# Kernel tuning notes

Hardware: AMD Instinct MI355X
Metric: run time of the kernel (lower is better)

The kernel has to match this reference:

```python
import jax, jax.numpy as jnp
import numpy as np

N, E, G = 50000, 800000, 512
EMB, HID, NSHAPE, NCOLOR, NCLS = 128, 256, 64, 64, 32


def setup_inputs() -> dict:
    key = jax.random.key(0)
    ks = jax.random.split(key, 12)
    s = 0.05
    return {
        "x": jax.random.randint(ks[0], (N, 2), 0, NSHAPE),
        "edge_index": jax.random.randint(ks[1], (2, E), 0, N),
        "batch": jnp.sort(jax.random.randint(ks[2], (N,), 0, G)),
        "shape_emb": jax.random.normal(ks[3], (NSHAPE, EMB)) * s,
        "color_emb": jax.random.normal(ks[4], (NCOLOR, EMB)) * s,
        # SAGEConv: lin_l (applied to aggregated neighbors, with bias), lin_r (root, no bias)
        "w1l": jax.random.normal(ks[5], (HID, 2 * EMB)) * s,
        "b1l": jnp.zeros((HID,)),
        "w1r": jax.random.normal(ks[6], (HID, 2 * EMB)) * s,
        "w2l": jax.random.normal(ks[7], (HID, HID)) * s,
        "b2l": jnp.zeros((HID,)),
        "w2r": jax.random.normal(ks[8], (HID, HID)) * s,
        "wc": jax.random.normal(ks[9], (NCLS, HID)) * s,
        "bc": jnp.zeros((NCLS,)),
    }


def _sage_conv(h, src, dst, wl, bl, wr):
    # mean-aggregate messages h[src] onto dst, then lin_l(aggr) + lin_r(h)
    msg = h[src]  # [E, d]
    agg = jax.ops.segment_sum(msg, dst, num_segments=N)  # [N, d]
    deg = jax.ops.segment_sum(jnp.ones((src.shape[0],), h.dtype), dst, num_segments=N)
    agg = agg / jnp.maximum(deg, 1.0)[:, None]
    return agg @ wl.T + bl + h @ wr.T


def reference(x, edge_index, batch, shape_emb, color_emb,
              w1l, b1l, w1r, w2l, b2l, w2r, wc, bc):
    src, dst = edge_index[0], edge_index[1]
    h = jnp.concatenate([shape_emb[x[:, 0]], color_emb[x[:, 1]]], axis=-1)  # [N, 2*EMB]
    h = jax.nn.relu(_sage_conv(h, src, dst, w1l, b1l, w1r))
    h = jax.nn.relu(_sage_conv(h, src, dst, w2l, b2l, w2r))
    # global mean pool over graphs
    hs = jax.ops.segment_sum(h, batch, num_segments=G)  # [G, HID]
    cnt = jax.ops.segment_sum(jnp.ones((N,), h.dtype), batch, num_segments=G)
    hg = hs / jnp.maximum(cnt, 1.0)[:, None]
    return hg @ wc.T + bc  # [G, NCLS]
```

## Files before the change

### kernel.cpp

```cpp
#include <hip/hip_runtime.h>
#include <hip/hip_bf16.h>


#define EMB   128
#define HID   256
#define NCLS  32
#define DIM   256

typedef __attribute__((ext_vector_type(8))) short short8v;
typedef __attribute__((ext_vector_type(4))) float float4v;

__device__ __forceinline__ unsigned short f2bf(float f) {
    unsigned int u = __float_as_uint(f);
    unsigned int r = u + 0x7FFFu + ((u >> 16) & 1u);
    return (unsigned short)(r >> 16);
}
__device__ __forceinline__ float bf2f(unsigned short s) {
    return __uint_as_float(((unsigned int)s) << 16);
}

__global__ void build_bq(const float* __restrict__ wl, const float* __restrict__ wr,
                         unsigned short* __restrict__ bhi, unsigned short* __restrict__ blo) {
    int tid = blockIdx.x * 256 + threadIdx.x;
    int k = tid >> 8, o = tid & 255;
    float v = (k < 256) ? wl[o * 256 + k] : wr[o * 256 + (k - 256)];
    unsigned short h = f2bf(v);
    unsigned short l = f2bf(v - bf2f(h));
    int idx = (((k >> 3) * 256) + o) * 8 + (k & 7);
    bhi[idx] = h;
    blo[idx] = l;
}

__global__ void embed_bf16(const int* __restrict__ x,
                           const float* __restrict__ se, const float* __restrict__ ce,
                           unsigned short* __restrict__ hb, int n_nodes) {
    int tid = blockIdx.x * 256 + threadIdx.x;
    if (tid >= n_nodes * 32) return;
    int n = tid >> 5, c = tid & 31;
    const float* src = (c < 16) ? (se + (size_t)x[n * 2] * EMB + c * 8)
                                : (ce + (size_t)x[n * 2 + 1] * EMB + (c - 16) * 8);
    float4 v0 = *(const float4*)src;
    float4 v1 = *(const float4*)(src + 4);
    ushort4 o0 = make_ushort4(f2bf(v0.x), f2bf(v0.y), f2bf(v0.z), f2bf(v0.w));
    ushort4 o1 = make_ushort4(f2bf(v1.x), f2bf(v1.y), f2bf(v1.z), f2bf(v1.w));
    *(ushort4*)(hb + (size_t)tid * 8)     = o0;
    *(ushort4*)(hb + (size_t)tid * 8 + 4) = o1;
}


__global__ void count_deg(const int* __restrict__ dst, int* __restrict__ deg, int E) {
    int e = blockIdx.x * 256 + threadIdx.x;
    if (e < E) atomicAdd(&deg[dst[e]], 1);
}

__global__ void scan_block(const int* __restrict__ deg, int* __restrict__ rowptr,
                           int* __restrict__ bsums, int n) {
    __shared__ int s[256];
    int t = threadIdx.x;
    int i = blockIdx.x * 256 + t;
    int v = (i < n) ? deg[i] : 0;
    s[t] = v; __syncthreads();
    for (int off = 1; off < 256; off <<= 1) {
        int x = (t >= off) ? s[t - off] : 0;
        __syncthreads(); s[t] += x; __syncthreads();
    }
    if (i < n) rowptr[i] = s[t] - v;
    if (t == 255) bsums[blockIdx.x] = s[255];
}

__global__ void scan_sums(int* __restrict__ bsums, int nb, int* __restrict__ rowptr,
                          int n, int E) {
    __shared__ int s[256];
    int t = threadIdx.x;
    int v = (t < nb) ? bsums[t] : 0;
    s[t] = v; __syncthreads();
    for (int off = 1; off < 256; off <<= 1) {
        int x = (t >= off) ? s[t - off] : 0;
        __syncthreads(); s[t] += x; __syncthreads();
    }
    if (t < nb) bsums[t] = s[t] - v;
    if (t == 0) rowptr[n] = E;
}

__global__ void scan_add(int* __restrict__ rowptr, const int* __restrict__ bsums, int n) {
    int i = blockIdx.x * 256 + threadIdx.x;
    if (i < n) rowptr[i] += bsums[i >> 8];
}

__global__ void fill_csr(const int* __restrict__ src, const int* __restrict__ dst,
                         const int* __restrict__ rowptr, int* __restrict__ cursor,
                         int* __restrict__ csr, int E) {
    int e = blockIdx.x * 256 + threadIdx.x;
    if (e >= E) return;
    int d = dst[e];
    int pos = rowptr[d] + atomicAdd(&cursor[d], 1);
    csr[pos] = src[e];
}

__global__ void aggregate_bf16(const unsigned short* __restrict__ hb,
                               const int* __restrict__ rowptr, const int* __restrict__ csr,
                               float* __restrict__ agg, int n_nodes) {
    int wid = (blockIdx.x * 256 + threadIdx.x) >> 6;
    int lane = threadIdx.x & 63;
    if (wid >= n_nodes) return;
    int beg = rowptr[wid], end = rowptr[wid + 1];
    float a0 = 0.f, a1 = 0.f, a2 = 0.f, a3 = 0.f;
    int k = beg;
    for (; k + 3 < end; k += 4) {
        int s0 = csr[k], s1 = csr[k + 1], s2 = csr[k + 2], s3 = csr[k + 3];
        ushort4 u0 = *(const ushort4*)(hb + (size_t)s0 * DIM + lane * 4);
        ushort4 u1 = *(const ushort4*)(hb + (size_t)s1 * DIM + lane * 4);
        ushort4 u2 = *(const ushort4*)(hb + (size_t)s2 * DIM + lane * 4);
        ushort4 u3 = *(const ushort4*)(hb + (size_t)s3 * DIM + lane * 4);
        a0 += bf2f(u0.x) + bf2f(u1.x) + bf2f(u2.x) + bf2f(u3.x);
        a1 += bf2f(u0.y) + bf2f(u1.y) + bf2f(u2.y) + bf2f(u3.y);
        a2 += bf2f(u0.z) + bf2f(u1.z) + bf2f(u2.z) + bf2f(u3.z);
        a3 += bf2f(u0.w) + bf2f(u1.w) + bf2f(u2.w) + bf2f(u3.w);
    }
    for (; k < end; ++k) {
        ushort4 u = *(const ushort4*)(hb + (size_t)csr[k] * DIM + lane * 4);
        a0 += bf2f(u.x); a1 += bf2f(u.y); a2 += bf2f(u.z); a3 += bf2f(u.w);
    }
    int d = end - beg;
    float inv = 1.0f / (float)(d > 1 ? d : 1);
    float4 o; o.x = a0 * inv; o.y = a1 * inv; o.z = a2 * inv; o.w = a3 * inv;
    *(float4*)(agg + (size_t)wid * DIM + lane * 4) = o;
}

__global__ void __launch_bounds__(256)
gemm_mfma(const float* __restrict__ Agg, const unsigned short* __restrict__ Hinb,
          const unsigned short* __restrict__ Bhi, const unsigned short* __restrict__ Blo,
          const float* __restrict__ bias,
          float* __restrict__ Houtf, unsigned short* __restrict__ Houtb, int M) {
    __shared__ __align__(16) unsigned short As_hi[64 * 40];
    __shared__ __align__(16) unsigned short As_lo[64 * 40];

    const int t = threadIdx.x;
    const int w = t >> 6, lane = t & 63;
    const int lrow = lane & 15, koct = lane >> 4;
    const int nw = w * 64;
    const int m0 = blockIdx.x * 64;

    float4v acc[4][4];
#pragma unroll
    for (int i = 0; i < 4; ++i)
#pragma unroll
        for (int j = 0; j < 4; ++j) acc[i][j] = (float4v){0.f, 0.f, 0.f, 0.f};

    const int sr = t >> 2;
    const int sc = (t & 3) * 8;
    const int gr = m0 + sr;
    const bool valid = (gr < M);

#pragma unroll 1
    for (int kt = 0; kt < 8; ++kt) {
        const float* __restrict__ Ap = Agg + (size_t)gr * DIM + (kt * 32 + sc);
        float4 v0 = make_float4(0.f, 0.f, 0.f, 0.f), v1 = v0;
        if (valid) { v0 = *(const float4*)Ap; v1 = *(const float4*)(Ap + 4); }
        float fv[8] = {v0.x, v0.y, v0.z, v0.w, v1.x, v1.y, v1.z, v1.w};
        unsigned short hs[8], ls[8];
#pragma unroll
        for (int i = 0; i < 8; ++i) {
            hs[i] = f2bf(fv[i]);
            ls[i] = f2bf(fv[i] - bf2f(hs[i]));
        }
        *(ushort4*)&As_hi[sr * 40 + sc]     = make_ushort4(hs[0], hs[1], hs[2], hs[3]);
        *(ushort4*)&As_hi[sr * 40 + sc + 4] = make_ushort4(hs[4], hs[5], hs[6], hs[7]);
        *(ushort4*)&As_lo[sr * 40 + sc]     = make_ushort4(ls[0], ls[1], ls[2], ls[3]);
        *(ushort4*)&As_lo[sr * 40 + sc + 4] = make_ushort4(ls[4], ls[5], ls[6], ls[7]);
        __syncthreads();

        const int kg = kt * 4 + koct;
        short8v bh[4], bl[4], ah[4], al[4];
#pragma unroll
        for (int nt = 0; nt < 4; ++nt) {
            size_t bofs = ((size_t)kg * 256 + (nw + nt * 16 + lrow)) * 8;
            bh[nt] = *(const short8v*)(Bhi + bofs);
            bl[nt] = *(const short8v*)(Blo + bofs);
        }
#pragma unroll
        for (int mt = 0; mt < 4; ++mt) {
            int aofs = (mt * 16 + lrow) * 40 + koct * 8;
            ah[mt] = *(const short8v*)&As_hi[aofs];
            al[mt] = *(const short8v*)&As_lo[aofs];
        }
#pragma unroll
        for (int mt = 0; mt < 4; ++mt)
#pragma unroll
            for (int nt = 0; nt < 4; ++nt) {
                acc[mt][nt] = __builtin_amdgcn_mfma_f32_16x16x32_bf16(ah[mt], bh[nt], acc[mt][nt], 0, 0, 0);
                acc[mt][nt] = __builtin_amdgcn_mfma_f32_16x16x32_bf16(ah[mt], bl[nt], acc[mt][nt], 0, 0, 0);
                acc[mt][nt] = __builtin_amdgcn_mfma_f32_16x16x32_bf16(al[mt], bh[nt], acc[mt][nt], 0, 0, 0);
            }
        __syncthreads();
    }

#pragma unroll 1
    for (int kt = 8; kt < 16; ++kt) {
        const unsigned short* __restrict__ Hp =
            Hinb + (size_t)gr * DIM + ((kt - 8) * 32 + sc);
        short8v hv = (short8v){0,0,0,0,0,0,0,0};
        if (valid) hv = *(const short8v*)Hp;
        *(short8v*)&As_hi[sr * 40 + sc] = hv;
        __syncthreads();

        const int kg = kt * 4 + koct;
        short8v bh[4], bl[4], ah[4];
#pragma unroll
        for (int nt = 0; nt < 4; ++nt) {
            size_t bofs = ((size_t)kg * 256 + (nw + nt * 16 + lrow)) * 8;
            bh[nt] = *(const short8v*)(Bhi + bofs);
            bl[nt] = *(const short8v*)(Blo + bofs);
        }
#pragma unroll
        for (int mt = 0; mt < 4; ++mt)
            ah[mt] = *(const short8v*)&As_hi[(mt * 16 + lrow) * 40 + koct * 8];
#pragma unroll
        for (int mt = 0; mt < 4; ++mt)
#pragma unroll
            for (int nt = 0; nt < 4; ++nt) {
                acc[mt][nt] = __builtin_amdgcn_mfma_f32_16x16x32_bf16(ah[mt], bh[nt], acc[mt][nt], 0, 0, 0);
                acc[mt][nt] = __builtin_amdgcn_mfma_f32_16x16x32_bf16(ah[mt], bl[nt], acc[mt][nt], 0, 0, 0);
            }
        __syncthreads();
    }

    float bv[4];
#pragma unroll
    for (int nt = 0; nt < 4; ++nt) bv[nt] = bias[nw + nt * 16 + lrow];

#pragma unroll
    for (int mt = 0; mt < 4; ++mt) {
#pragma unroll
        for (int r = 0; r < 4; ++r) {
            int grow = m0 + mt * 16 + koct * 4 + r;
            if (grow >= M) continue;
#pragma unroll
            for (int nt = 0; nt < 4; ++nt) {
                float vv = fmaxf(acc[mt][nt][r] + bv[nt], 0.f);
                int col = nw + nt * 16 + lrow;
                if (Houtf) Houtf[(size_t)grow * DIM + col] = vv;
                if (Houtb) Houtb[(size_t)grow * DIM + col] = f2bf(vv);
            }
        }
    }
}


__global__ void pool_kernel(const float* __restrict__ h, const int* __restrict__ batch,
                            float* __restrict__ hg, int n_nodes) {
    int g = blockIdx.x;
    int t = threadIdx.x;
    int lo = 0, hi = n_nodes;
    while (lo < hi) { int mid = (lo + hi) >> 1; if (batch[mid] < g) lo = mid + 1; else hi = mid; }
    int start = lo;
    hi = n_nodes;
    while (lo < hi) { int mid = (lo + hi) >> 1; if (batch[mid] < g + 1) lo = mid + 1; else hi = mid; }
    int end = lo;
    float acc = 0.f;
    for (int n = start; n < end; ++n) acc += h[(size_t)n * DIM + t];
    int c = end - start;
    hg[g * DIM + t] = acc / (float)(c > 1 ? c : 1);
}

__global__ void head_kernel(const float* __restrict__ hg, const float* __restrict__ wc,
                            const float* __restrict__ bc, float* __restrict__ out, int total) {
    int tid = blockIdx.x * 256 + threadIdx.x;
    if (tid >= total) return;
    int g = tid >> 5, c = tid & 31;
    const float* hr = hg + (size_t)g * DIM;
    const float* wr = wc + (size_t)c * DIM;
    float acc = bc[c];
    for (int k = 0; k < DIM; ++k) acc = fmaf(hr[k], wr[k], acc);
    out[tid] = acc;
}


extern "C" void kernel_launch(void* const* d_in, const int* in_sizes, int n_in,
                              void* d_out, int out_size, void* d_ws, size_t ws_size,
                              hipStream_t stream) {
    const int* x      = (const int*)d_in[0];
    const int* ei     = (const int*)d_in[1];
    const int* batch  = (const int*)d_in[2];
    const float* se   = (const float*)d_in[3];
    const float* ce   = (const float*)d_in[4];
    const float* w1l  = (const float*)d_in[5];
    const float* b1l  = (const float*)d_in[6];
    const float* w1r  = (const float*)d_in[7];
    const float* w2l  = (const float*)d_in[8];
    const float* b2l  = (const float*)d_in[9];
    const float* w2r  = (const float*)d_in[10];
    const float* wc   = (const float*)d_in[11];
    const float* bc   = (const float*)d_in[12];
    float* out = (float*)d_out;

    const int N = in_sizes[0] / 2;
    const int E = in_sizes[1] / 2;
    const int G = out_size / NCLS;
    const int* src = ei;
    const int* dst = ei + E;

    float* agg = (float*)d_ws;
    float* h2  = agg + (size_t)N * DIM;
    unsigned short* h0b = (unsigned short*)(h2 + (size_t)N * DIM);
    unsigned short* h1b = h0b + (size_t)N * DIM;
    unsigned short* B1hi = h1b + (size_t)N * DIM;
    unsigned short* B1lo = B1hi + 131072;
    unsigned short* B2hi = B1lo + 131072;
    unsigned short* B2lo = B2hi + 131072;
    float* hg  = (float*)(B2lo + 131072);
    int* deg    = (int*)(hg + (size_t)G * DIM);
    int* rowptr = deg + N;
    int* cursor = rowptr + (N + 1);
    int* csr    = cursor + N;
    int* bsums  = csr + E;

    hipMemsetAsync(deg, 0, (size_t)(3 * N + 1) * sizeof(int), stream);

    embed_bf16<<<(N * 32 + 255) / 256, 256, 0, stream>>>(x, se, ce, h0b, N);

    int eblocks = (E + 255) / 256;
    count_deg<<<eblocks, 256, 0, stream>>>(dst, deg, E);
    int sblocks = (N + 255) / 256;
    scan_block<<<sblocks, 256, 0, stream>>>(deg, rowptr, bsums, N);
    scan_sums<<<1, 256, 0, stream>>>(bsums, sblocks, rowptr, N, E);
    scan_add<<<sblocks, 256, 0, stream>>>(rowptr, bsums, N);
    fill_csr<<<eblocks, 256, 0, stream>>>(src, dst, rowptr, cursor, csr, E);

    build_bq<<<512, 256, 0, stream>>>(w1l, w1r, B1hi, B1lo);
    build_bq<<<512, 256, 0, stream>>>(w2l, w2r, B2hi, B2lo);

    int gblocks = (N + 63) / 64;
    int ablocks = (N * 64 + 255) / 256;

    aggregate_bf16<<<ablocks, 256, 0, stream>>>(h0b, rowptr, csr, agg, N);
    gemm_mfma<<<gblocks, 256, 0, stream>>>(agg, h0b, B1hi, B1lo, b1l, nullptr, h1b, N);

    aggregate_bf16<<<ablocks, 256, 0, stream>>>(h1b, rowptr, csr, agg, N);
    gemm_mfma<<<gblocks, 256, 0, stream>>>(agg, h1b, B2hi, B2lo, b2l, h2, nullptr, N);

    pool_kernel<<<G, 256, 0, stream>>>(h2, batch, hg, N);
    head_kernel<<<(G * NCLS + 255) / 256, 256, 0, stream>>>(hg, wc, bc, out, G * NCLS);
}
```

Measured before the change: 462.0 us.

## Split aggregate into bf16 hi/lo in producer and load GEMM A directly from global

The aggregation kernel now writes the mean-aggregated features as bf16 hi/lo pairs instead of fp32, moving the split-precision conversion out of the GEMM. The GEMM drops its shared-memory staging and barriers, loading A fragments for MFMA straight from global memory with clamped row indices, and unrolls its k loops by two. The two weight-packing launches are merged into one. Global A reads are now strided per lane and each of the four waves re-reads the same A rows, so the gain depends on cache hits. The aggregate output stays the same size in bytes.

Measured after the change: 495.9 us. +7.3%, slower.

```diff
diff --git a/kernel.cpp b/kernel.cpp
--- a/kernel.cpp
+++ b/kernel.cpp
@@ -19,16 +19,22 @@
     return __uint_as_float(((unsigned int)s) << 16);
 }
 
-__global__ void build_bq(const float* __restrict__ wl, const float* __restrict__ wr,
-                         unsigned short* __restrict__ bhi, unsigned short* __restrict__ blo) {
+__global__ void build_bq2(const float* __restrict__ w1l, const float* __restrict__ w1r,
+                          const float* __restrict__ w2l, const float* __restrict__ w2r,
+                          unsigned short* __restrict__ b1hi, unsigned short* __restrict__ b1lo,
+                          unsigned short* __restrict__ b2hi, unsigned short* __restrict__ b2lo) {
     int tid = blockIdx.x * 256 + threadIdx.x;
-    int k = tid >> 8, o = tid & 255;
+    int which = tid >> 17;
+    int r = tid & 0x1FFFF;
+    int k = r >> 8, o = r & 255;
+    const float* wl = which ? w2l : w1l;
+    const float* wr = which ? w2r : w1r;
     float v = (k < 256) ? wl[o * 256 + k] : wr[o * 256 + (k - 256)];
     unsigned short h = f2bf(v);
     unsigned short l = f2bf(v - bf2f(h));
     int idx = (((k >> 3) * 256) + o) * 8 + (k & 7);
-    bhi[idx] = h;
-    blo[idx] = l;
+    (which ? b2hi : b1hi)[idx] = h;
+    (which ? b2lo : b1lo)[idx] = l;
 }
 
 __global__ void embed_bf16(const int* __restrict__ x,
@@ -99,7 +105,8 @@
 
 __global__ void aggregate_bf16(const unsigned short* __restrict__ hb,
                                const int* __restrict__ rowptr, const int* __restrict__ csr,
-                               float* __restrict__ agg, int n_nodes) {
+                               unsigned short* __restrict__ ahi, unsigned short* __restrict__ alo,
+                               int n_nodes) {
     int wid = (blockIdx.x * 256 + threadIdx.x) >> 6;
     int lane = threadIdx.x & 63;
     if (wid >= n_nodes) return;
@@ -123,55 +130,52 @@
     }
     int d = end - beg;
     float inv = 1.0f / (float)(d > 1 ? d : 1);
-    float4 o; o.x = a0 * inv; o.y = a1 * inv; o.z = a2 * inv; o.w = a3 * inv;
-    *(float4*)(agg + (size_t)wid * DIM + lane * 4) = o;
+    float v[4] = {a0 * inv, a1 * inv, a2 * inv, a3 * inv};
+    unsigned short hs[4], ls[4];
+#pragma unroll
+    for (int i = 0; i < 4; ++i) {
+        hs[i] = f2bf(v[i]);
+        ls[i] = f2bf(v[i] - bf2f(hs[i]));
+    }
+    *(ushort4*)(ahi + (size_t)wid * DIM + lane * 4) = make_ushort4(hs[0], hs[1], hs[2], hs[3]);
+    *(ushort4*)(alo + (size_t)wid * DIM + lane * 4) = make_ushort4(ls[0], ls[1], ls[2], ls[3]);
 }
 
 __global__ void __launch_bounds__(256)
-gemm_mfma(const float* __restrict__ Agg, const unsigned short* __restrict__ Hinb,
+gemm_mfma(const unsigned short* __restrict__ Ahi, const unsigned short* __restrict__ Alo,
+          const unsigned short* __restrict__ Hinb,
           const unsigned short* __restrict__ Bhi, const unsigned short* __restrict__ Blo,
           const float* __restrict__ bias,
           float* __restrict__ Houtf, unsigned short* __restrict__ Houtb, int M) {
-    __shared__ __align__(16) unsigned short As_hi[64 * 40];
-    __shared__ __align__(16) unsigned short As_lo[64 * 40];
-
     const int t = threadIdx.x;
     const int w = t >> 6, lane = t & 63;
     const int lrow = lane & 15, koct = lane >> 4;
     const int nw = w * 64;
     const int m0 = blockIdx.x * 64;
 
+    size_t arow[4];
+#pragma unroll
+    for (int mt = 0; mt < 4; ++mt) {
+        int r = m0 + mt * 16 + lrow;
+        arow[mt] = (size_t)(r < M ? r : M - 1) * DIM;
+    }
+
     float4v acc[4][4];
 #pragma unroll
     for (int i = 0; i < 4; ++i)
 #pragma unroll
         for (int j = 0; j < 4; ++j) acc[i][j] = (float4v){0.f, 0.f, 0.f, 0.f};
 
-    const int sr = t >> 2;
-    const int sc = (t & 3) * 8;
-    const int gr = m0 + sr;
-    const bool valid = (gr < M);
-
-#pragma unroll 1
+#pragma unroll 2
     for (int kt = 0; kt < 8; ++kt) {
-        const float* __restrict__ Ap = Agg + (size_t)gr * DIM + (kt * 32 + sc);
-        float4 v0 = make_float4(0.f, 0.f, 0.f, 0.f), v1 = v0;
-        if (valid) { v0 = *(const float4*)Ap; v1 = *(const float4*)(Ap + 4); }
-        float fv[8] = {v0.x, v0.y, v0.z, v0.w, v1.x, v1.y, v1.z, v1.w};
-        unsigned short hs[8], ls[8];
-#pragma unroll
-        for (int i = 0; i < 8; ++i) {
-            hs[i] = f2bf(fv[i]);
-            ls[i] = f2bf(fv[i] - bf2f(hs[i]));
+        const int kofs = kt * 32 + koct * 8;
+        const int kg = kt * 4 + koct;
+        short8v ah[4], al[4], bh[4], bl[4];
+#pragma unroll
+        for (int mt = 0; mt < 4; ++mt) {
+            ah[mt] = *(const short8v*)(Ahi + arow[mt] + kofs);
+            al[mt] = *(const short8v*)(Alo + arow[mt] + kofs);
         }
-        *(ushort4*)&As_hi[sr * 40 + sc]     = make_ushort4(hs[0], hs[1], hs[2], hs[3]);
-        *(ushort4*)&As_hi[sr * 40 + sc + 4] = make_ushort4(hs[4], hs[5], hs[6], hs[7]);
-        *(ushort4*)&As_lo[sr * 40 + sc]     = make_ushort4(ls[0], ls[1], ls[2], ls[3]);
-        *(ushort4*)&As_lo[sr * 40 + sc + 4] = make_ushort4(ls[4], ls[5], ls[6], ls[7]);
-        __syncthreads();
-
-        const int kg = kt * 4 + koct;
-        short8v bh[4], bl[4], ah[4], al[4];
 #pragma unroll
         for (int nt = 0; nt < 4; ++nt) {
             size_t bofs = ((size_t)kg * 256 + (nw + nt * 16 + lrow)) * 8;
@@ -179,12 +183,6 @@
             bl[nt] = *(const short8v*)(Blo + bofs);
         }
 #pragma unroll
-        for (int mt = 0; mt < 4; ++mt) {
-            int aofs = (mt * 16 + lrow) * 40 + koct * 8;
-            ah[mt] = *(const short8v*)&As_hi[aofs];
-            al[mt] = *(const short8v*)&As_lo[aofs];
-        }
-#pragma unroll
         for (int mt = 0; mt < 4; ++mt)
 #pragma unroll
             for (int nt = 0; nt < 4; ++nt) {
@@ -192,20 +190,16 @@
                 acc[mt][nt] = __builtin_amdgcn_mfma_f32_16x16x32_bf16(ah[mt], bl[nt], acc[mt][nt], 0, 0, 0);
                 acc[mt][nt] = __builtin_amdgcn_mfma_f32_16x16x32_bf16(al[mt], bh[nt], acc[mt][nt], 0, 0, 0);
             }
-        __syncthreads();
-    }
-
-#pragma unroll 1
-    for (int kt = 8; kt < 16; ++kt) {
-        const unsigned short* __restrict__ Hp =
-            Hinb + (size_t)gr * DIM + ((kt - 8) * 32 + sc);
-        short8v hv = (short8v){0,0,0,0,0,0,0,0};
-        if (valid) hv = *(const short8v*)Hp;
-        *(short8v*)&As_hi[sr * 40 + sc] = hv;
-        __syncthreads();
-
-        const int kg = kt * 4 + koct;
-        short8v bh[4], bl[4], ah[4];
+    }
+
+#pragma unroll 2
+    for (int kt = 0; kt < 8; ++kt) {
+        const int kofs = kt * 32 + koct * 8;
+        const int kg = (kt + 8) * 4 + koct;
+        short8v ah[4], bh[4], bl[4];
+#pragma unroll
+        for (int mt = 0; mt < 4; ++mt)
+            ah[mt] = *(const short8v*)(Hinb + arow[mt] + kofs);
 #pragma unroll
         for (int nt = 0; nt < 4; ++nt) {
             size_t bofs = ((size_t)kg * 256 + (nw + nt * 16 + lrow)) * 8;
@@ -214,15 +208,11 @@
         }
 #pragma unroll
         for (int mt = 0; mt < 4; ++mt)
-            ah[mt] = *(const short8v*)&As_hi[(mt * 16 + lrow) * 40 + koct * 8];
-#pragma unroll
-        for (int mt = 0; mt < 4; ++mt)
 #pragma unroll
             for (int nt = 0; nt < 4; ++nt) {
                 acc[mt][nt] = __builtin_amdgcn_mfma_f32_16x16x32_bf16(ah[mt], bh[nt], acc[mt][nt], 0, 0, 0);
                 acc[mt][nt] = __builtin_amdgcn_mfma_f32_16x16x32_bf16(ah[mt], bl[nt], acc[mt][nt], 0, 0, 0);
             }
-        __syncthreads();
     }
 
     float bv[4];
@@ -300,14 +290,15 @@
     const int* src = ei;
     const int* dst = ei + E;
 
-    float* agg = (float*)d_ws;
-    float* h2  = agg + (size_t)N * DIM;
-    unsigned short* h0b = (unsigned short*)(h2 + (size_t)N * DIM);
-    unsigned short* h1b = h0b + (size_t)N * DIM;
-    unsigned short* B1hi = h1b + (size_t)N * DIM;
-    unsigned short* B1lo = B1hi + 131072;
-    unsigned short* B2hi = B1lo + 131072;
-    unsigned short* B2lo = B2hi + 131072;
+    float* h2 = (float*)d_ws;
+    unsigned short* agghi = (unsigned short*)(h2 + (size_t)N * DIM);
+    unsigned short* agglo = agghi + (size_t)N * DIM;
+    unsigned short* h0b   = agglo + (size_t)N * DIM;
+    unsigned short* h1b   = h0b + (size_t)N * DIM;
+    unsigned short* B1hi  = h1b + (size_t)N * DIM;
+    unsigned short* B1lo  = B1hi + 131072;
+    unsigned short* B2hi  = B1lo + 131072;
+    unsigned short* B2lo  = B2hi + 131072;
     float* hg  = (float*)(B2lo + 131072);
     int* deg    = (int*)(hg + (size_t)G * DIM);
     int* rowptr = deg + N;
@@ -327,17 +318,16 @@
     scan_add<<<sblocks, 256, 0, stream>>>(rowptr, bsums, N);
     fill_csr<<<eblocks, 256, 0, stream>>>(src, dst, rowptr, cursor, csr, E);
 
-    build_bq<<<512, 256, 0, stream>>>(w1l, w1r, B1hi, B1lo);
-    build_bq<<<512, 256, 0, stream>>>(w2l, w2r, B2hi, B2lo);
+    build_bq2<<<1024, 256, 0, stream>>>(w1l, w1r, w2l, w2r, B1hi, B1lo, B2hi, B2lo);
 
     int gblocks = (N + 63) / 64;
     int ablocks = (N * 64 + 255) / 256;
 
-    aggregate_bf16<<<ablocks, 256, 0, stream>>>(h0b, rowptr, csr, agg, N);
-    gemm_mfma<<<gblocks, 256, 0, stream>>>(agg, h0b, B1hi, B1lo, b1l, nullptr, h1b, N);
-
-    aggregate_bf16<<<ablocks, 256, 0, stream>>>(h1b, rowptr, csr, agg, N);
-    gemm_mfma<<<gblocks, 256, 0, stream>>>(agg, h1b, B2hi, B2lo, b2l, h2, nullptr, N);
+    aggregate_bf16<<<ablocks, 256, 0, stream>>>(h0b, rowptr, csr, agghi, agglo, N);
+    gemm_mfma<<<gblocks, 256, 0, stream>>>(agghi, agglo, h0b, B1hi, B1lo, b1l, nullptr, h1b, N);
+
+    aggregate_bf16<<<ablocks, 256, 0, stream>>>(h1b, rowptr, csr, agghi, agglo, N);
+    gemm_mfma<<<gblocks, 256, 0, stream>>>(agghi, agglo, h1b, B2hi, B2lo, b2l, h2, nullptr, N);
 
     pool_kernel<<<G, 256, 0, stream>>>(h2, batch, hg, N);
     head_kernel<<<(G * NCLS + 255) / 256, 256, 0, stream>>>(hg, wc, bc, out, G * NCLS);
```
